# Performance work log

Hardware: AMD Instinct MI355X
Metric: run time of the kernel (lower is better)

## Reference

```python
import jax, jax.numpy as jnp
import numpy as np

T, H, F, E, K, C = 8192, 1024, 2048, 16, 2, 1280  # tokens, hidden, ffn, experts, top_k, capacity


def setup_inputs() -> dict:
    key = jax.random.key(0)
    ks = jax.random.split(key, 6)
    return {
        "x": jax.random.normal(ks[0], (T, H), dtype=jnp.float32),
        "w_router": jax.random.normal(ks[1], (H, E), dtype=jnp.float32) * 0.02,
        "w1": jax.random.normal(ks[2], (E, H, F), dtype=jnp.float32) * 0.02,
        "b1": jnp.zeros((E, F), dtype=jnp.float32),
        "w2": jax.random.normal(ks[3], (E, F, H), dtype=jnp.float32) * 0.02,
        "b2": jnp.zeros((E, H), dtype=jnp.float32),
    }


def reference(x, w_router, w1, b1, w2, b2):
    # ---- Router: softmax + top-k (TopKRouter) ----
    logits = x @ w_router                                  # [T, E]
    probs = jax.nn.softmax(logits, axis=-1)
    topk_p, topk_idx = jax.lax.top_k(probs, K)             # [T, K]
    topk_p = topk_p / jnp.sum(topk_p, axis=-1, keepdims=True)

    # ---- Dispatch with capacity drop (token_permutation) ----
    flat_e = topk_idx.reshape(-1)                          # [T*K] expert id per assignment
    token_ids = jnp.repeat(jnp.arange(T), K)               # [T*K]
    oh = jax.nn.one_hot(flat_e, E, dtype=jnp.int32)        # [T*K, E]
    # position of each assignment within its expert's buffer (token order)
    pos = jnp.cumsum(oh, axis=0) - oh                      # [T*K, E]
    pos = jnp.take_along_axis(pos, flat_e[:, None], axis=1)[:, 0]  # [T*K]
    keep = pos < C
    safe_pos = jnp.where(keep, pos, C)                     # dropped tokens -> dummy slot C

    dispatched = jnp.zeros((E, C + 1, H), dtype=x.dtype)
    dispatched = dispatched.at[flat_e, safe_pos].add(x[token_ids])
    disp = dispatched[:, :C, :]                            # [E, C, H]

    # ---- Grouped expert MLP (SequentialMLP: fc1 -> gelu -> fc2) ----
    h = jax.nn.gelu(jnp.einsum("ech,ehf->ecf", disp, w1) + b1[:, None, :])
    y = jnp.einsum("ecf,efh->ech", h, w2) + b2[:, None, :]  # [E, C, H]

    # ---- Combine (token_unpermutation): gather + prob-weighted sum ----
    y_pad = jnp.pad(y, ((0, 0), (0, 1), (0, 0)))            # dummy slot returns garbage, masked below
    gathered = y_pad[flat_e, safe_pos]                      # [T*K, H]
    gathered = jnp.where(keep[:, None], gathered, 0.0)
    weighted = gathered * topk_p.reshape(-1)[:, None]
    out = jax.ops.segment_sum(weighted, token_ids, num_segments=T)  # [T, H]
    return out
```

## Files before the change

kernel.cpp:

```cpp
#include <hip/hip_runtime.h>
#include <cstdint>
#include <cstddef>

#define T_TOK 8192
#define HDIM  1024
#define FDIM  2048
#define NEXP  16
#define CAP   1280

typedef __bf16 bf16x8 __attribute__((ext_vector_type(8)));
typedef float  f32x4  __attribute__((ext_vector_type(4)));

__device__ inline void gld16(const void* g, void* l) {
  __builtin_amdgcn_global_load_lds(
      (__attribute__((address_space(1))) void*)g,
      (__attribute__((address_space(3))) void*)l, 16, 0, 0);
}

__global__ __launch_bounds__(256) void router_kernel(
    const float* __restrict__ x, const float* __restrict__ wr,
    int* __restrict__ eidx, float* __restrict__ eprob) {
  int t = blockIdx.x * 4 + (threadIdx.x >> 6);
  int lane = threadIdx.x & 63;
  float acc[NEXP];
#pragma unroll
  for (int e = 0; e < NEXP; ++e) acc[e] = 0.f;
  const float4* xp = (const float4*)(x + (size_t)t * HDIM + lane * 16);
#pragma unroll
  for (int q = 0; q < 4; ++q) {
    float4 xv = xp[q];
    float xa[4] = {xv.x, xv.y, xv.z, xv.w};
#pragma unroll
    for (int ii = 0; ii < 4; ++ii) {
      int h = lane * 16 + q * 4 + ii;
      const float4* wp = (const float4*)(wr + (size_t)h * NEXP);
      float w[NEXP];
      float4 w0 = wp[0], w1 = wp[1], w2 = wp[2], w3 = wp[3];
      w[0]=w0.x; w[1]=w0.y; w[2]=w0.z; w[3]=w0.w;
      w[4]=w1.x; w[5]=w1.y; w[6]=w1.z; w[7]=w1.w;
      w[8]=w2.x; w[9]=w2.y; w[10]=w2.z; w[11]=w2.w;
      w[12]=w3.x; w[13]=w3.y; w[14]=w3.z; w[15]=w3.w;
#pragma unroll
      for (int e = 0; e < NEXP; ++e) acc[e] += xa[ii] * w[e];
    }
  }
#pragma unroll
  for (int e = 0; e < NEXP; ++e) {
#pragma unroll
    for (int s = 32; s > 0; s >>= 1) acc[e] += __shfl_xor(acc[e], s);
  }
  if (lane == 0) {
    float l0 = -1e30f, l1 = -1e30f; int i0 = 0, i1 = 0;
#pragma unroll
    for (int e = 0; e < NEXP; ++e) {
      float v = acc[e];
      if (v > l0) { l1 = l0; i1 = i0; l0 = v; i0 = e; }
      else if (v > l1) { l1 = v; i1 = e; }
    }
    float p0 = 1.f / (1.f + __expf(l1 - l0));
    eidx[t * 2 + 0] = i0; eidx[t * 2 + 1] = i1;
    eprob[t * 2 + 0] = p0; eprob[t * 2 + 1] = 1.f - p0;
  }
}

__global__ __launch_bounds__(256) void pos_kernel(
    const int* __restrict__ eidx, const float* __restrict__ eprob,
    int* __restrict__ slot_token, float* __restrict__ slot_prob) {
  __shared__ int scan[256][NEXP];
  int tid = threadIdx.x;
  int cnt[NEXP];
#pragma unroll
  for (int e = 0; e < NEXP; ++e) cnt[e] = 0;
  int base_i = tid * 64;
  const int4* ep = (const int4*)(eidx + base_i);
  for (int i = 0; i < 16; ++i) {
    int4 v = ep[i];
    cnt[v.x]++; cnt[v.y]++; cnt[v.z]++; cnt[v.w]++;
  }
#pragma unroll
  for (int e = 0; e < NEXP; ++e) scan[tid][e] = cnt[e];
  __syncthreads();
  if (tid < NEXP) {
    int run = 0;
    for (int i = 0; i < 256; ++i) { int v = scan[i][tid]; scan[i][tid] = run; run += v; }
  }
  __syncthreads();
  int basec[NEXP];
#pragma unroll
  for (int e = 0; e < NEXP; ++e) basec[e] = scan[tid][e];
  for (int i = 0; i < 64; ++i) {
    int fi = base_i + i;
    int e = eidx[fi];
    int p = basec[e]++;
    if (p < CAP) {
      slot_token[e * CAP + p] = fi >> 1;
      slot_prob[e * CAP + p] = eprob[fi];
    }
  }
}

__global__ __launch_bounds__(256) void scatter_kernel(
    const float* __restrict__ x, const int* __restrict__ slot_token,
    __bf16* __restrict__ disp) {
  int s = blockIdx.x * 4 + (threadIdx.x >> 6);
  int lane = threadIdx.x & 63;
  int tok = slot_token[s];
  __bf16 vals[16] __attribute__((aligned(16)));
  if (tok >= 0) {
    const float4* xp = (const float4*)(x + (size_t)tok * HDIM + lane * 16);
#pragma unroll
    for (int q = 0; q < 4; ++q) {
      float4 v = xp[q];
      vals[q * 4 + 0] = (__bf16)v.x; vals[q * 4 + 1] = (__bf16)v.y;
      vals[q * 4 + 2] = (__bf16)v.z; vals[q * 4 + 3] = (__bf16)v.w;
    }
  } else {
#pragma unroll
    for (int q = 0; q < 16; ++q) vals[q] = (__bf16)0.f;
  }
  uint4* dst = (uint4*)(disp + (size_t)s * HDIM + lane * 16);
  dst[0] = ((uint4*)vals)[0];
  dst[1] = ((uint4*)vals)[1];
}

__global__ __launch_bounds__(256) void transpose_cast_kernel(
    const float* __restrict__ src, __bf16* __restrict__ dst, int R, int Cc) {
  int e = blockIdx.z;
  src += (size_t)e * R * Cc;
  dst += (size_t)e * R * Cc;
  __shared__ float tile[64][65];
  int gy = blockIdx.y * 64;
  int gx = blockIdx.x * 64;
  int tid = threadIdx.x;
  int r = tid >> 4;
  int c4 = (tid & 15) * 4;
#pragma unroll
  for (int rr = 0; rr < 4; ++rr) {
    float4 v = *(const float4*)(src + (size_t)(gy + r + rr * 16) * Cc + gx + c4);
    tile[r + rr * 16][c4 + 0] = v.x;
    tile[r + rr * 16][c4 + 1] = v.y;
    tile[r + rr * 16][c4 + 2] = v.z;
    tile[r + rr * 16][c4 + 3] = v.w;
  }
  __syncthreads();
  int r2 = tid >> 2;
  int cb = (tid & 3) * 16;
  __bf16 o[16] __attribute__((aligned(16)));
#pragma unroll
  for (int i = 0; i < 16; ++i) o[i] = (__bf16)tile[cb + i][r2];
  uint4* dp = (uint4*)(dst + (size_t)(gx + r2) * R + gy + cb);
  dp[0] = ((uint4*)o)[0];
  dp[1] = ((uint4*)o)[1];
}

template <int EPI, int KSPLIT>
__global__ __launch_bounds__(512, 2) void moe_gemm_kernel(
    const __bf16* __restrict__ A, const __bf16* __restrict__ Bt,
    const float* __restrict__ bias, __bf16* __restrict__ Hout,
    const int* __restrict__ slot_token, const float* __restrict__ slot_prob,
    float* __restrict__ out, int M, int N, int Kd) {
  const int e  = blockIdx.z / KSPLIT;
  const int ks = blockIdx.z % KSPLIT;
  const int m0 = blockIdx.y * 256, n0 = blockIdx.x * 256;
  const char* Ae = (const char*)A + (size_t)e * M * Kd * 2;
  const char* Be = (const char*)Bt + (size_t)e * N * Kd * 2;
  __shared__ __bf16 lds[2 * 32768];
  const int tid = threadIdx.x, wave = tid >> 6, lane = tid & 63;
  const int quad = lane >> 4, l15 = lane & 15;
  const int wm = (wave >> 2) * 128, wn = (wave & 3) * 64;
  f32x4 acc[8][4] = {};
  const size_t Kb = (size_t)Kd * 2;
  const int ktiles = (Kd / KSPLIT) >> 6;
  const int kbase = ks * (Kd / KSPLIT) * 2;

  const int rbase = tid >> 3;
  const int scol  = ((tid & 7) ^ ((tid >> 3) & 7)) * 16;
  const char* srcA = Ae + (size_t)(m0 + rbase) * Kb + kbase + scol;
  const char* srcB = Be + (size_t)(n0 + rbase) * Kb + kbase + scol;
  const size_t rstep = 64 * Kb;
  const int dofs = tid * 16;

  auto stage = [&](int t) {
    char* base = (char*)lds + (t & 1) * 65536;
#pragma unroll
    for (int j = 0; j < 4; ++j)
      gld16(srcA + (size_t)t * 128 + j * rstep, base + dofs + j * 8192);
#pragma unroll
    for (int j = 0; j < 4; ++j)
      gld16(srcB + (size_t)t * 128 + j * rstep, base + 32768 + dofs + j * 8192);
  };

  int aoff[8], boff[4], coff[2];
#pragma unroll
  for (int i = 0; i < 8; ++i) aoff[i] = (wm + i * 16 + l15) * 128;
#pragma unroll
  for (int j = 0; j < 4; ++j) boff[j] = (wn + j * 16 + l15) * 128;
#pragma unroll
  for (int kk = 0; kk < 2; ++kk) coff[kk] = (((kk * 4 + quad) ^ (l15 & 7)) * 16);

  stage(0);
  __builtin_amdgcn_s_waitcnt(0x0f70);
  __builtin_amdgcn_s_barrier();
  for (int t = 0; t < ktiles; ++t) {
    if (t + 1 < ktiles) stage(t + 1);
    const char* La = (const char*)lds + (t & 1) * 65536;
    const char* Lb = La + 32768;
#pragma unroll
    for (int kk = 0; kk < 2; ++kk) {
      bf16x8 av[8], bv[4];
#pragma unroll
      for (int i = 0; i < 8; ++i) av[i] = *(const bf16x8*)(La + aoff[i] + coff[kk]);
#pragma unroll
      for (int j = 0; j < 4; ++j) bv[j] = *(const bf16x8*)(Lb + boff[j] + coff[kk]);
      __builtin_amdgcn_s_setprio(1);
#pragma unroll
      for (int i = 0; i < 8; ++i)
#pragma unroll
        for (int j = 0; j < 4; ++j)
          acc[i][j] = __builtin_amdgcn_mfma_f32_16x16x32_bf16(av[i], bv[j], acc[i][j], 0, 0, 0);
      __builtin_amdgcn_s_setprio(0);
    }
    if (t + 1 < ktiles) __builtin_amdgcn_s_waitcnt(0x0f70);
    __builtin_amdgcn_s_barrier();
  }
  if (EPI == 1) {
    __bf16* He = Hout + (size_t)e * M * N;
    float bj[4];
#pragma unroll
    for (int j = 0; j < 4; ++j) bj[j] = bias[(size_t)e * N + n0 + wn + j * 16 + l15];
#pragma unroll
    for (int i = 0; i < 8; ++i) {
#pragma unroll
      for (int r = 0; r < 4; ++r) {
        int m = m0 + wm + i * 16 + quad * 4 + r;
#pragma unroll
        for (int j = 0; j < 4; ++j) {
          int n = n0 + wn + j * 16 + l15;
          float v = acc[i][j][r] + bj[j];
          float u = 0.7978845608028654f * (v + 0.044715f * v * v * v);
          float ex = __expf(-2.f * fabsf(u));
          float th = (1.f - ex) / (1.f + ex);
          th = copysignf(th, u);
          He[(size_t)m * N + n] = (__bf16)(0.5f * v * (1.f + th));
        }
      }
    }
  } else {
    const int* st = slot_token + e * CAP;
    const float* sp = slot_prob + e * CAP;
    float bj[4];
#pragma unroll
    for (int j = 0; j < 4; ++j)
      bj[j] = (ks == 0) ? bias[(size_t)e * N + n0 + wn + j * 16 + l15] : 0.f;
#pragma unroll
    for (int i = 0; i < 8; ++i) {
#pragma unroll
      for (int r = 0; r < 4; ++r) {
        int m = m0 + wm + i * 16 + quad * 4 + r;
        int tok = st[m];
        if (tok >= 0) {
          float p = sp[m];
#pragma unroll
          for (int j = 0; j < 4; ++j) {
            int n = n0 + wn + j * 16 + l15;
            float v = acc[i][j][r] + bj[j];
            atomicAdd(out + (size_t)tok * HDIM + n, p * v);
          }
        }
      }
    }
  }
}

extern "C" void kernel_launch(void* const* d_in, const int* in_sizes, int n_in,
                              void* d_out, int out_size, void* d_ws, size_t ws_size,
                              hipStream_t stream) {
  const float* x  = (const float*)d_in[0];
  const float* wr = (const float*)d_in[1];
  const float* w1 = (const float*)d_in[2];
  const float* b1 = (const float*)d_in[3];
  const float* w2 = (const float*)d_in[4];
  const float* b2 = (const float*)d_in[5];
  float* out = (float*)d_out;

  char* ws = (char*)d_ws;
  size_t off = 0;
  __bf16* w1t = (__bf16*)(ws + off); off += (size_t)NEXP * FDIM * HDIM * 2;
  __bf16* w2t = (__bf16*)(ws + off); off += (size_t)NEXP * HDIM * FDIM * 2;
  __bf16* disp = (__bf16*)(ws + off); off += (size_t)NEXP * CAP * HDIM * 2;
  __bf16* hbuf = (__bf16*)(ws + off); off += (size_t)NEXP * CAP * FDIM * 2;
  int*   slot_token = (int*)(ws + off);  off += (size_t)NEXP * CAP * 4;
  float* slot_prob  = (float*)(ws + off); off += (size_t)NEXP * CAP * 4;
  int*   eidx  = (int*)(ws + off);  off += (size_t)T_TOK * 2 * 4;
  float* eprob = (float*)(ws + off); off += (size_t)T_TOK * 2 * 4;
  if (ws_size < off) return;

  hipMemsetAsync(slot_token, 0xFF, (size_t)NEXP * CAP * 4, stream);
  hipMemsetAsync(d_out, 0, (size_t)T_TOK * HDIM * 4, stream);

  transpose_cast_kernel<<<dim3(FDIM / 64, HDIM / 64, NEXP), 256, 0, stream>>>(w1, w1t, HDIM, FDIM);
  transpose_cast_kernel<<<dim3(HDIM / 64, FDIM / 64, NEXP), 256, 0, stream>>>(w2, w2t, FDIM, HDIM);

  router_kernel<<<T_TOK / 4, 256, 0, stream>>>(x, wr, eidx, eprob);
  pos_kernel<<<1, 256, 0, stream>>>(eidx, eprob, slot_token, slot_prob);
  scatter_kernel<<<NEXP * CAP / 4, 256, 0, stream>>>(x, slot_token, disp);

  moe_gemm_kernel<1, 1><<<dim3(FDIM / 256, CAP / 256, NEXP), 512, 0, stream>>>(
      disp, w1t, b1, hbuf, nullptr, nullptr, nullptr, CAP, FDIM, HDIM);
  moe_gemm_kernel<2, 2><<<dim3(HDIM / 256, CAP / 256, NEXP * 2), 512, 0, stream>>>(
      hbuf, w2t, b2, nullptr, slot_token, slot_prob, out, CAP, HDIM, FDIM);
}
```

Baseline: 780.2 us.

## Store GEMM operands in K-tiled slabs and remap workgroups across XCDs

All GEMM operands (dispatched activations, transposed weights, and the intermediate H) are now stored in a K-blocked layout: 64-wide K slabs, each holding contiguous 128-byte rows. Each stage's global-to-LDS load then reads one contiguous chunk instead of rows strided by the full K dimension. The GEMM kernel also remaps its flat workgroup index so that consecutive tiles land on the same XCD, which is meant to improve L2 reuse. The cost is that producers write with more scattered addresses, and every kernel has to agree on the new layout.

Measured after the change: 754.9 us. 1.03x faster.

```diff
diff --git a/kernel.cpp b/kernel.cpp
--- a/kernel.cpp
+++ b/kernel.cpp
@@ -104,6 +104,7 @@
     __bf16* __restrict__ disp) {
   int s = blockIdx.x * 4 + (threadIdx.x >> 6);
   int lane = threadIdx.x & 63;
+  int e = s / CAP, m = s % CAP;
   int tok = slot_token[s];
   __bf16 vals[16] __attribute__((aligned(16)));
   if (tok >= 0) {
@@ -118,7 +119,7 @@
 #pragma unroll
     for (int q = 0; q < 16; ++q) vals[q] = (__bf16)0.f;
   }
-  uint4* dst = (uint4*)(disp + (size_t)s * HDIM + lane * 16);
+  uint4* dst = (uint4*)(disp + (((size_t)e * 16 + (lane >> 2)) * CAP + m) * 64 + (lane & 3) * 16);
   dst[0] = ((uint4*)vals)[0];
   dst[1] = ((uint4*)vals)[1];
 }
@@ -148,7 +149,7 @@
   __bf16 o[16] __attribute__((aligned(16)));
 #pragma unroll
   for (int i = 0; i < 16; ++i) o[i] = (__bf16)tile[cb + i][r2];
-  uint4* dp = (uint4*)(dst + (size_t)(gx + r2) * R + gy + cb);
+  uint4* dp = (uint4*)(dst + ((size_t)(gy >> 6) * Cc + gx + r2) * 64 + cb);
   dp[0] = ((uint4*)o)[0];
   dp[1] = ((uint4*)o)[1];
 }
@@ -159,35 +160,44 @@
     const float* __restrict__ bias, __bf16* __restrict__ Hout,
     const int* __restrict__ slot_token, const float* __restrict__ slot_prob,
     float* __restrict__ out, int M, int N, int Kd) {
-  const int e  = blockIdx.z / KSPLIT;
-  const int ks = blockIdx.z % KSPLIT;
-  const int m0 = blockIdx.y * 256, n0 = blockIdx.x * 256;
-  const char* Ae = (const char*)A + (size_t)e * M * Kd * 2;
-  const char* Be = (const char*)Bt + (size_t)e * N * Kd * 2;
+  const int nwg = gridDim.x * gridDim.y * gridDim.z;
+  int flat = (blockIdx.z * gridDim.y + blockIdx.y) * gridDim.x + blockIdx.x;
+  flat = (flat & 7) * (nwg >> 3) + (flat >> 3);
+  const int bx = flat % gridDim.x;
+  int tmpf = flat / gridDim.x;
+  const int by = tmpf % gridDim.y;
+  const int bz = tmpf / gridDim.y;
+
+  const int e  = bz / KSPLIT;
+  const int ks = bz % KSPLIT;
+  const int m0 = by * 256, n0 = bx * 256;
   __shared__ __bf16 lds[2 * 32768];
   const int tid = threadIdx.x, wave = tid >> 6, lane = tid & 63;
   const int quad = lane >> 4, l15 = lane & 15;
   const int wm = (wave >> 2) * 128, wn = (wave & 3) * 64;
   f32x4 acc[8][4] = {};
-  const size_t Kb = (size_t)Kd * 2;
   const int ktiles = (Kd / KSPLIT) >> 6;
-  const int kbase = ks * (Kd / KSPLIT) * 2;
+  const size_t slabA = (size_t)M * 128;
+  const size_t slabB = (size_t)N * 128;
 
   const int rbase = tid >> 3;
-  const int scol  = ((tid & 7) ^ ((tid >> 3) & 7)) * 16;
-  const char* srcA = Ae + (size_t)(m0 + rbase) * Kb + kbase + scol;
-  const char* srcB = Be + (size_t)(n0 + rbase) * Kb + kbase + scol;
-  const size_t rstep = 64 * Kb;
+  const int swz = ((tid & 7) ^ (rbase & 7)) * 16;
+  const char* srcA = (const char*)A + (size_t)e * (Kd >> 6) * slabA
+                     + (size_t)(m0 + rbase) * 128 + swz;
+  const char* srcB = (const char*)Bt + (size_t)e * (Kd >> 6) * slabB
+                     + (size_t)(n0 + rbase) * 128 + swz;
   const int dofs = tid * 16;
 
   auto stage = [&](int t) {
     char* base = (char*)lds + (t & 1) * 65536;
+    const char* sA = srcA + (size_t)(ks * ktiles + t) * slabA;
+    const char* sB = srcB + (size_t)(ks * ktiles + t) * slabB;
 #pragma unroll
     for (int j = 0; j < 4; ++j)
-      gld16(srcA + (size_t)t * 128 + j * rstep, base + dofs + j * 8192);
+      gld16(sA + j * 8192, base + dofs + j * 8192);
 #pragma unroll
     for (int j = 0; j < 4; ++j)
-      gld16(srcB + (size_t)t * 128 + j * rstep, base + 32768 + dofs + j * 8192);
+      gld16(sB + j * 8192, base + 32768 + dofs + j * 8192);
   };
 
   int aoff[8], boff[4], coff[2];
@@ -225,6 +235,7 @@
   }
   if (EPI == 1) {
     __bf16* He = Hout + (size_t)e * M * N;
+    const size_t kfbase = (size_t)((n0 + wn) >> 6) * M;
     float bj[4];
 #pragma unroll
     for (int j = 0; j < 4; ++j) bj[j] = bias[(size_t)e * N + n0 + wn + j * 16 + l15];
@@ -235,13 +246,12 @@
         int m = m0 + wm + i * 16 + quad * 4 + r;
 #pragma unroll
         for (int j = 0; j < 4; ++j) {
-          int n = n0 + wn + j * 16 + l15;
           float v = acc[i][j][r] + bj[j];
           float u = 0.7978845608028654f * (v + 0.044715f * v * v * v);
           float ex = __expf(-2.f * fabsf(u));
           float th = (1.f - ex) / (1.f + ex);
           th = copysignf(th, u);
-          He[(size_t)m * N + n] = (__bf16)(0.5f * v * (1.f + th));
+          He[(kfbase + m) * 64 + j * 16 + l15] = (__bf16)(0.5f * v * (1.f + th));
         }
       }
     }
```
